# Optimization experiments

Hardware: AMD Instinct MI355X
Metric: run time of the kernel (lower is better)

## Reference

```python
import jax, jax.numpy as jnp
import numpy as np
from functools import partial

# ---- NASA Li-ion battery default parameters (Daigle model) ----
P = {}
P['qMobile'] = 7600.0
P['xnMax'] = 0.6; P['xnMin'] = 0.0
P['xpMax'] = 1.0; P['xpMin'] = 0.4
P['qmax'] = P['qMobile'] / (P['xnMax'] - P['xnMin'])  # 12666.667
P['Ro'] = 0.117215
P['R'] = 8.3144621
P['F'] = 96487.0
P['alpha'] = 0.5
P['Sn'] = 0.000437545
P['Sp'] = 0.00030962
P['kn'] = 2120.96
P['kp'] = 248898.0
P['Volume'] = 2e-5
P['VolumeSurf'] = 0.1
P['tDiffusion'] = 7e6
P['to'] = 6.08671
P['tsn'] = 1001.38
P['tsp'] = 46.4311
P['VolS'] = P['VolumeSurf'] * P['Volume']
P['VolB'] = P['Volume'] - P['VolS']
P['qSMax'] = P['qmax'] * P['VolS'] / P['Volume']
P['qBMax'] = P['qmax'] * P['VolB'] / P['Volume']
U0P, U0N = 4.03, 0.01
APS = np.array([-31593.7, 0.106747, 24606.4, -78561.9, 13317.9, 307387.0,
                84916.1, -1.07469e6, 2285.04, 990894.0, 283920.0, -161513.0,
                -469218.0], dtype=np.float32)
ANS = np.array([86.19], dtype=np.float32)
DT = 1.0
B, T = 2048, 1024


def _vint(x, As, F):
    N = As.shape[0]
    k = jnp.arange(N, dtype=x.dtype)          # [N]
    ki = jnp.arange(N)
    b = (2.0 * x - 1.0)[..., None]            # [B,1]
    ab, sg = jnp.abs(b), jnp.sign(b)
    # integer-exponent pow with correct sign for negative base
    p_kp1 = ab ** (k + 1.0) * jnp.where((ki + 1) % 2 == 1, sg, 1.0)
    p_km1 = ab ** (k - 1.0) * jnp.where((ki - 1) % 2 != 0, sg, 1.0)
    term = p_kp1 - (2.0 * x * (1.0 - x))[..., None] * k * p_km1
    return (term @ As) / F


def _vint_safe(x, As, F):
    ok = x != 0.5
    sx = jnp.where(ok, x, 1.0)
    return jnp.where(ok, _vint(sx, As, F), 0.0)


def _step(state, i, Aps, Ans):
    tb, Vo, Vsn, Vsp, qnB, qnS, qpB, qpS = state
    R, F, alpha = P['R'], P['F'], P['alpha']
    xpS = qpS / P['qSMax']
    xnS = qnS / P['qSMax']
    Jn0 = P['kn'] * (1.0 - xnS) ** alpha * xnS ** alpha
    Jp0 = P['kp'] * (1.0 - xpS) ** alpha * xpS ** alpha
    dBSn = (qnB / P['VolB'] - qnS / P['VolS']) / P['tDiffusion']
    dBSp = (qpB / P['VolB'] - qpS / P['VolS']) / P['tDiffusion']
    Jn, Jp = i / P['Sn'], i / P['Sp']
    VoN = i * P['Ro']
    VsnN = R * tb / (F * alpha) * jnp.arcsinh(Jn / (2.0 * Jn0))
    VspN = R * tb / (F * alpha) * jnp.arcsinh(Jp / (2.0 * Jp0))
    Ven = U0N + R * tb / F * jnp.log((1.0 - xnS) / xnS) + _vint_safe(xnS, Ans, F)
    Vep = U0P + R * tb / F * jnp.log((1.0 - xpS) / xpS) + _vint_safe(xpS, Aps, F)
    v = Vep - Ven - Vo - Vsn - Vsp
    new = (tb,
           Vo + DT * (VoN - Vo) / P['to'],
           Vsn + DT * (VsnN - Vsn) / P['tsn'],
           Vsp + DT * (VspN - Vsp) / P['tsp'],
           qnB - DT * dBSn,
           qnS + DT * (dBSn - i),
           qpB - DT * dBSp,
           qpS + DT * (i + dBSp))
    return new, v


def setup_inputs() -> dict:
    key = jax.random.key(0)
    k1, = jax.random.split(key, 1)
    i = 0.1 + 0.9 * jax.random.uniform(k1, (B, T), dtype=jnp.float32)  # amps
    qnS0 = P['xnMax'] * P['qmax'] * P['VolS'] / P['Volume']
    qnB0 = P['xnMax'] * P['qmax'] * P['VolB'] / P['Volume']
    qpS0 = P['xpMin'] * P['qmax'] * P['VolS'] / P['Volume']
    qpB0 = P['xpMin'] * P['qmax'] * P['VolB'] / P['Volume']
    x0 = jnp.tile(jnp.array([292.1, 0.0, 0.0, 0.0, qnB0, qnS0, qpB0, qpS0],
                            dtype=jnp.float32), (B, 1))
    return {'i': i, 'x0': x0, 'Aps': jnp.asarray(APS), 'Ans': jnp.asarray(ANS)}


def reference(i, x0, Aps, Ans):
    state0 = tuple(x0[:, j] for j in range(8))
    def body(st, it):
        return _step(st, it, Aps, Ans)
    _, v = jax.lax.scan(body, state0, i.T)  # v: [T,B]
    return v.T  # voltage per cell per step, [B,T]
```

## Files before the change

kernel.cpp:

```cpp
#include <hip/hip_runtime.h>
#include <math.h>


constexpr int NTHR = 256;
constexpr int L = 4;
constexpr int NW = NTHR / 64;

__global__ __launch_bounds__(NTHR, 6) void battery_scan2(
    const float* __restrict__ I, const float* __restrict__ X0,
    const float* __restrict__ Aps, const float* __restrict__ Ans,
    float* __restrict__ out, int Tn)
{
    const int cell = blockIdx.x;
    const int tid  = threadIdx.x;
    const int lane = tid & 63;
    const int wv   = tid >> 6;

    __shared__ float shA[3][NW];
    __shared__ float shC[2][NW];

    const float ivB    = (float)(1.0/1.8e-5);
    const float ivS    = (float)(1.0/2.0e-6);
    const float invSum = (float)(1.0/(1.0/1.8e-5 + 1.0/2.0e-6));
    const float aq     = (float)(1.0 - (1.0/1.8e-5 + 1.0/2.0e-6)/7.0e6);
    const float ao     = (float)(1.0 - 1.0/6.08671);
    const float asn    = (float)(1.0 - 1.0/1001.38);
    const float asp    = (float)(1.0 - 1.0/46.4311);
    const float inv_qS = (float)(1.0/1266.6666666666667);
    const float invF   = (float)(1.0/96487.0);
    const float c_zn   = (float)(0.5/0.000437545/2120.96);
    const float c_zp   = (float)(0.5/0.00030962/248898.0);
    const float Ro_to  = (float)(0.117215/6.08671);
    const float inv_tsn= (float)(1.0/1001.38);
    const float inv_tsp= (float)(1.0/46.4311);
    const float U0PN   = 4.03f - 0.01f;

    const float aqp[4]  = {1.f, aq,  aq*aq,   aq*aq*aq};
    const float aop[4]  = {1.f, ao,  ao*ao,   ao*ao*ao};
    const float asnp[4] = {1.f, asn, asn*asn, asn*asn*asn};
    const float aspp[4] = {1.f, asp, asp*asp, asp*asp*asp};
    const float aq4 = aqp[3]*aq, ao4 = aop[3]*ao;
    const float asn4 = asnp[3]*asn, asp4 = aspp[3]*asp;

    const float tb   = X0[cell*8+0];
    const float Vo0  = X0[cell*8+1];
    const float Vsn0 = X0[cell*8+2];
    const float Vsp0 = X0[cell*8+3];
    const float qnB0 = X0[cell*8+4];
    const float qnS0 = X0[cell*8+5];
    const float qpB0 = X0[cell*8+6];
    const float qpS0 = X0[cell*8+7];
    const float An0  = Ans[0];

    const float rtf  = 8.3144621f * tb * invF;
    const float rtfa = 2.f*rtf;
    const float u_n0 = qnB0 + qnS0;
    const float u_p0 = qpB0 + qpS0;
    const float w_n0 = qnB0*ivB - qnS0*ivS;
    const float w_p0 = qpB0*ivB - qpS0*ivS;

    const float fl = (float)lane;
    const float plq  = exp2f(fl * __log2f(aq4));
    const float plo  = exp2f(fl * __log2f(ao4));
    const float pln  = exp2f(fl * __log2f(asn4));
    const float plp  = exp2f(fl * __log2f(asp4));

    const float4 iv4 = *(const float4*)(I + (size_t)cell*Tn + tid*L);
    const float i4[4] = {iv4.x, iv4.y, iv4.z, iv4.w};

    auto wscan = [&](float tot, float R4, float& ep, float& Tw, float& R64) {
        float v = tot, r = R4;
        #pragma unroll
        for (int s = 1; s < 64; s <<= 1) {
            float p = __shfl_up(v, s);
            v = (lane >= s) ? fmaf(r, p, v) : v;
            r *= r;
        }
        float e = __shfl_up(v, 1);
        ep = (lane == 0) ? 0.f : e;
        Tw = __shfl(v, 63);
        R64 = r;
    };

    float es[4], eg[4], eo[4];
    float ts = 0.f, tg = 0.f, to_ = 0.f;
    #pragma unroll
    for (int k = 0; k < L; ++k) {
        es[k] = ts; eg[k] = tg; eo[k] = to_;
        float b = i4[k];
        ts  += b;
        tg   = fmaf(aq, tg, b);
        to_  = fmaf(ao, to_, b);
    }
    float epS, TwS, RS, epG, TwG, RG, epO, TwO, RO;
    wscan(ts,  1.f, epS, TwS, RS);
    wscan(tg,  aq4, epG, TwG, RG);
    wscan(to_, ao4, epO, TwO, RO);
    if (lane == 0) { shA[0][wv] = TwS; shA[1][wv] = TwG; shA[2][wv] = TwO; }
    __syncthreads();
    float Cs = 0.f, Cg = 0.f, Co = 0.f;
    for (int w2 = 0; w2 < wv; ++w2) {
        Cs = Cs + shA[0][w2];
        Cg = fmaf(RG, Cg, 0.f) ; Cg = Cg;
        Co = Co;
        (void)0;
    }
    Cs = 0.f; Cg = 0.f; Co = 0.f;
    for (int w2 = 0; w2 < wv; ++w2) {
        Cs = Cs + shA[0][w2];
        Cg = fmaf(Cg, RG, shA[1][w2]) - Cg*RG + Cg*RG;
        Co = Co*RO + shA[2][w2];
    }
    {
        Cs = 0.f; Cg = 0.f; Co = 0.f;
        #pragma unroll
        for (int w2 = 0; w2 < NW; ++w2) {
            if (w2 < wv) {
                Cs = Cs + shA[0][w2];
                Cg = Cg*RG + shA[1][w2];
                Co = Co*RO + shA[2][w2];
            }
        }
    }
    const float cs = epS + Cs;
    const float cg = fmaf(plq, Cg, epG);
    const float co = fmaf(plo, Co, epO);

    float pwq = plq, pwo = plo;
    for (int w2 = 0; w2 < wv; ++w2) { pwq *= RG; pwo *= RO; }

    float vpart[4], bsn[4], bsp[4];
    float tn_ = 0.f, tp_ = 0.f;
    #pragma unroll
    for (int k = 0; k < L; ++k) {
        float s_t = cs + es[k];
        float g_t = fmaf(aqp[k], cg, eg[k]);
        float o_t = fmaf(aop[k], co, eo[k]);
        float u_n = u_n0 - s_t, u_p = u_p0 + s_t;
        float paq = pwq * aqp[k];
        float w_n = fmaf(paq, w_n0,  ivS*g_t);
        float w_p = fmaf(paq, w_p0, -ivS*g_t);
        float qnS = (u_n*ivB - w_n)*invSum;
        float qpS = (u_p*ivB - w_p)*invSum;
        float xnS = qnS*inv_qS, xpS = qpS*inv_qS;
        float Vo_t = fmaf(pwo*aop[k], Vo0, Ro_to*o_t);
        float it = i4[k];

        float pn = xnS*(1.f - xnS);
        float pp = xpS*(1.f - xpS);
        float zn = it * c_zn * rsqrtf(pn);
        float zp = it * c_zp * rsqrtf(pp);
        float VsnN = rtfa*__logf(zn + sqrtf(fmaf(zn, zn, 1.f)));
        float VspN = rtfa*__logf(zp + sqrtf(fmaf(zp, zp, 1.f)));

        float num = (1.f - xpS)*xnS;
        float den = xpS*(1.f - xnS);
        float lr  = __logf(__fdividef(num, den));

        float bp_ = 2.f*xpS - 1.f;
        float P = 0.f, D = 0.f;
        #pragma unroll
        for (int j = 12; j >= 0; --j) {
            D = fmaf(D, bp_, P);
            P = fmaf(P, bp_, Aps[j]);
        }
        float vint_p = (xpS != 0.5f)
                     ? (bp_*P - 2.f*xpS*(1.f - xpS)*D)*invF : 0.f;
        float bn_ = 2.f*xnS - 1.f;
        float vint_n = (xnS != 0.5f) ? An0*bn_*invF : 0.f;

        vpart[k] = U0PN + rtf*lr + vint_p - vint_n - Vo_t;
        float bn = VsnN * inv_tsn;
        float bpv = VspN * inv_tsp;
        bsn[k] = bn; bsp[k] = bpv;
        tn_ = fmaf(asn, tn_, bn);
        tp_ = fmaf(asp, tp_, bpv);
    }

    float epN, TwN, RN, epP, TwP, RP;
    wscan(tn_, asn4, epN, TwN, RN);
    wscan(tp_, asp4, epP, TwP, RP);
    if (lane == 0) { shC[0][wv] = TwN; shC[1][wv] = TwP; }
    __syncthreads();
    float Cn = 0.f, Cp = 0.f;
    #pragma unroll
    for (int w2 = 0; w2 < NW; ++w2) {
        if (w2 < wv) {
            Cn = Cn*RN + shC[0][w2];
            Cp = Cp*RP + shC[1][w2];
        }
    }
    const float csn = fmaf(pln, Cn, epN);
    const float csp = fmaf(plp, Cp, epP);
    float pwn = pln, pwp = plp;
    for (int w2 = 0; w2 < wv; ++w2) { pwn *= RN; pwp *= RP; }

    float res[4];
    float an_ = 0.f, ap_ = 0.f;
    #pragma unroll
    for (int k = 0; k < L; ++k) {
        float Vsn_t = fmaf(pwn*asnp[k], Vsn0, fmaf(asnp[k], csn, an_));
        float Vsp_t = fmaf(pwp*aspp[k], Vsp0, fmaf(aspp[k], csp, ap_));
        res[k] = vpart[k] - Vsn_t - Vsp_t;
        an_ = fmaf(asn, an_, bsn[k]);
        ap_ = fmaf(asp, ap_, bsp[k]);
    }
    *(float4*)(out + (size_t)cell*Tn + tid*L) = make_float4(res[0],res[1],res[2],res[3]);
}

extern "C" void kernel_launch(void* const* d_in, const int* in_sizes, int n_in,
                              void* d_out, int out_size, void* d_ws, size_t ws_size,
                              hipStream_t stream) {
    const float* I   = (const float*)d_in[0];
    const float* X0  = (const float*)d_in[1];
    const float* Aps = (const float*)d_in[2];
    const float* Ans = (const float*)d_in[3];
    float* out = (float*)d_out;

    int Bn = in_sizes[1] / 8;
    int Tn = in_sizes[0] / Bn;

    battery_scan2<<<dim3(Bn), dim3(NTHR), 0, stream>>>(I, X0, Aps, Ans, out, Tn);
}
```

Before: 74.66 us.

## Use 128-thread blocks with 8 steps per thread and incremental decay recurrences

Each block now covers a cell's 1024 steps with 2 waves instead of 4, and each thread handles 8 timesteps. That halves the number of shuffle-based wave scans per element and reduces the cross-wave combine to a single branch. Per-step decay powers are now updated by running multiplication instead of precomputed tables, and several constants are folded together. The positive-electrode arcsinh is replaced by a cubic Taylor series, which assumes the argument stays small. Longer serial chains per thread and higher register pressure may lower latency hiding.

```diff
diff --git a/kernel.cpp b/kernel.cpp
--- a/kernel.cpp
+++ b/kernel.cpp
@@ -2,11 +2,10 @@
 #include <math.h>
 
 
-constexpr int NTHR = 256;
-constexpr int L = 4;
-constexpr int NW = NTHR / 64;
+constexpr int NTHR = 128;
+constexpr int L = 8;
 
-__global__ __launch_bounds__(NTHR, 6) void battery_scan2(
+__global__ __launch_bounds__(NTHR, 4) void battery_scan3(
     const float* __restrict__ I, const float* __restrict__ X0,
     const float* __restrict__ Aps, const float* __restrict__ Ans,
     float* __restrict__ out, int Tn)
@@ -16,31 +15,27 @@
     const int lane = tid & 63;
     const int wv   = tid >> 6;
 
-    __shared__ float shA[3][NW];
-    __shared__ float shC[2][NW];
+    __shared__ float shA[3][2];
+    __shared__ float shC[2][2];
 
     const float ivB    = (float)(1.0/1.8e-5);
     const float ivS    = (float)(1.0/2.0e-6);
-    const float invSum = (float)(1.0/(1.0/1.8e-5 + 1.0/2.0e-6));
     const float aq     = (float)(1.0 - (1.0/1.8e-5 + 1.0/2.0e-6)/7.0e6);
     const float ao     = (float)(1.0 - 1.0/6.08671);
     const float asn    = (float)(1.0 - 1.0/1001.38);
     const float asp    = (float)(1.0 - 1.0/46.4311);
-    const float inv_qS = (float)(1.0/1266.6666666666667);
+    const float invSum = (float)(1.0/(1.0/1.8e-5 + 1.0/2.0e-6));
+    const float cX     = (float)((1.0/(1.0/1.8e-5 + 1.0/2.0e-6)) / 1266.6666666666667);
     const float invF   = (float)(1.0/96487.0);
     const float c_zn   = (float)(0.5/0.000437545/2120.96);
     const float c_zp   = (float)(0.5/0.00030962/248898.0);
     const float Ro_to  = (float)(0.117215/6.08671);
-    const float inv_tsn= (float)(1.0/1001.38);
-    const float inv_tsp= (float)(1.0/46.4311);
     const float U0PN   = 4.03f - 0.01f;
 
-    const float aqp[4]  = {1.f, aq,  aq*aq,   aq*aq*aq};
-    const float aop[4]  = {1.f, ao,  ao*ao,   ao*ao*ao};
-    const float asnp[4] = {1.f, asn, asn*asn, asn*asn*asn};
-    const float aspp[4] = {1.f, asp, asp*asp, asp*asp*asp};
-    const float aq4 = aqp[3]*aq, ao4 = aop[3]*ao;
-    const float asn4 = asnp[3]*asn, asp4 = aspp[3]*asp;
+    float aqp = 1.f, aop = 1.f, asnp = 1.f, aspp = 1.f;
+    #pragma unroll
+    for (int k = 0; k < L; ++k) { aqp *= aq; aop *= ao; asnp *= asn; aspp *= asp; }
+    const float aqL = aqp, aoL = aop, asnL = asnp, aspL = aspp;
 
     const float tb   = X0[cell*8+0];
     const float Vo0  = X0[cell*8+1];
@@ -50,26 +45,30 @@
     const float qnS0 = X0[cell*8+5];
     const float qpB0 = X0[cell*8+6];
     const float qpS0 = X0[cell*8+7];
-    const float An0  = Ans[0];
+    const float An0F = Ans[0] * invF;
 
-    const float rtf  = 8.3144621f * tb * invF;
-    const float rtfa = 2.f*rtf;
-    const float u_n0 = qnB0 + qnS0;
-    const float u_p0 = qpB0 + qpS0;
-    const float w_n0 = qnB0*ivB - qnS0*ivS;
-    const float w_p0 = qpB0*ivB - qpS0*ivS;
+    const float rtf   = 8.3144621f * tb * invF;
+    const float rtfa  = 2.f*rtf;
+    const float bn_c  = rtfa * (float)(1.0/1001.38);
+    const float bp_c  = rtfa * (float)(1.0/46.4311);
+    const float u_n0  = qnB0 + qnS0;
+    const float u_p0  = qpB0 + qpS0;
+    const float w_n0  = qnB0*ivB - qnS0*ivS;
+    const float w_p0  = qpB0*ivB - qpS0*ivS;
 
     const float fl = (float)lane;
-    const float plq  = exp2f(fl * __log2f(aq4));
-    const float plo  = exp2f(fl * __log2f(ao4));
-    const float pln  = exp2f(fl * __log2f(asn4));
-    const float plp  = exp2f(fl * __log2f(asp4));
+    const float plq = exp2f(fl * __log2f(aqL));
+    const float plo = exp2f(fl * __log2f(aoL));
+    const float pln = exp2f(fl * __log2f(asnL));
+    const float plp = exp2f(fl * __log2f(aspL));
 
-    const float4 iv4 = *(const float4*)(I + (size_t)cell*Tn + tid*L);
-    const float i4[4] = {iv4.x, iv4.y, iv4.z, iv4.w};
+    const float* ibase = I + (size_t)cell*Tn + tid*L;
+    const float4 iva = *(const float4*)(ibase);
+    const float4 ivb = *(const float4*)(ibase + 4);
+    const float i8[8] = {iva.x, iva.y, iva.z, iva.w, ivb.x, ivb.y, ivb.z, ivb.w};
 
-    auto wscan = [&](float tot, float R4, float& ep, float& Tw, float& R64) {
-        float v = tot, r = R4;
+    auto wscan = [&](float tot, float RL, float& ep, float& Tw, float& R64) {
+        float v = tot, r = RL;
         #pragma unroll
         for (int s = 1; s < 64; s <<= 1) {
             float p = __shfl_up(v, s);
@@ -82,130 +81,100 @@
         R64 = r;
     };
 
-    float es[4], eg[4], eo[4];
     float ts = 0.f, tg = 0.f, to_ = 0.f;
     #pragma unroll
     for (int k = 0; k < L; ++k) {
-        es[k] = ts; eg[k] = tg; eo[k] = to_;
-        float b = i4[k];
-        ts  += b;
-        tg   = fmaf(aq, tg, b);
-        to_  = fmaf(ao, to_, b);
+        float b = i8[k];
+        ts += b; tg = fmaf(aq, tg, b); to_ = fmaf(ao, to_, b);
     }
     float epS, TwS, RS, epG, TwG, RG, epO, TwO, RO;
     wscan(ts,  1.f, epS, TwS, RS);
-    wscan(tg,  aq4, epG, TwG, RG);
-    wscan(to_, ao4, epO, TwO, RO);
+    wscan(tg,  aqL, epG, TwG, RG);
+    wscan(to_, aoL, epO, TwO, RO);
     if (lane == 0) { shA[0][wv] = TwS; shA[1][wv] = TwG; shA[2][wv] = TwO; }
     __syncthreads();
-    float Cs = 0.f, Cg = 0.f, Co = 0.f;
-    for (int w2 = 0; w2 < wv; ++w2) {
-        Cs = Cs + shA[0][w2];
-        Cg = fmaf(RG, Cg, 0.f) ; Cg = Cg;
-        Co = Co;
-        (void)0;
+    float cs = epS, cg = epG, co = epO;
+    float pwq = plq, pwo = plo;
+    if (wv) {
+        cs += shA[0][0];
+        cg = fmaf(plq, shA[1][0], cg);
+        co = fmaf(plo, shA[2][0], co);
+        pwq *= RG; pwo *= RO;
     }
-    Cs = 0.f; Cg = 0.f; Co = 0.f;
-    for (int w2 = 0; w2 < wv; ++w2) {
-        Cs = Cs + shA[0][w2];
-        Cg = fmaf(Cg, RG, shA[1][w2]) - Cg*RG + Cg*RG;
-        Co = Co*RO + shA[2][w2];
-    }
-    {
-        Cs = 0.f; Cg = 0.f; Co = 0.f;
-        #pragma unroll
-        for (int w2 = 0; w2 < NW; ++w2) {
-            if (w2 < wv) {
-                Cs = Cs + shA[0][w2];
-                Cg = Cg*RG + shA[1][w2];
-                Co = Co*RO + shA[2][w2];
-            }
-        }
-    }
-    const float cs = epS + Cs;
-    const float cg = fmaf(plq, Cg, epG);
-    const float co = fmaf(plo, Co, epO);
 
-    float pwq = plq, pwo = plo;
-    for (int w2 = 0; w2 < wv; ++w2) { pwq *= RG; pwo *= RO; }
-
-    float vpart[4], bsn[4], bsp[4];
-    float tn_ = 0.f, tp_ = 0.f;
+    float vpart[L], bsn[L], bsp[L];
+    float S = cs, G = cg, O = co;
+    float hwn = pwq*w_n0, hwp = pwq*w_p0;
+    float hvo = pwo*Vo0;
+    float rn = 0.f, rp = 0.f;
     #pragma unroll
     for (int k = 0; k < L; ++k) {
-        float s_t = cs + es[k];
-        float g_t = fmaf(aqp[k], cg, eg[k]);
-        float o_t = fmaf(aop[k], co, eo[k]);
-        float u_n = u_n0 - s_t, u_p = u_p0 + s_t;
-        float paq = pwq * aqp[k];
-        float w_n = fmaf(paq, w_n0,  ivS*g_t);
-        float w_p = fmaf(paq, w_p0, -ivS*g_t);
-        float qnS = (u_n*ivB - w_n)*invSum;
-        float qpS = (u_p*ivB - w_p)*invSum;
-        float xnS = qnS*inv_qS, xpS = qpS*inv_qS;
-        float Vo_t = fmaf(pwo*aop[k], Vo0, Ro_to*o_t);
-        float it = i4[k];
+        float it  = i8[k];
+        float u_n = u_n0 - S, u_p = u_p0 + S;
+        float w_n = fmaf( ivS, G, hwn);
+        float w_p = fmaf(-ivS, G, hwp);
+        float xnS = (fmaf(u_n, ivB, -w_n)) * cX;
+        float xpS = (fmaf(u_p, ivB, -w_p)) * cX;
+        float Vo_t = fmaf(Ro_to, O, hvo);
+        S += it; G = fmaf(aq, G, it); O = fmaf(ao, O, it);
+        hwn *= aq; hwp *= aq; hvo *= ao;
 
-        float pn = xnS*(1.f - xnS);
-        float pp = xpS*(1.f - xpS);
+        float pn = fmaf(-xnS, xnS, xnS);
+        float pp = fmaf(-xpS, xpS, xpS);
         float zn = it * c_zn * rsqrtf(pn);
         float zp = it * c_zp * rsqrtf(pp);
-        float VsnN = rtfa*__logf(zn + sqrtf(fmaf(zn, zn, 1.f)));
-        float VspN = rtfa*__logf(zp + sqrtf(fmaf(zp, zp, 1.f)));
+        float asn_n = __logf(zn + sqrtf(fmaf(zn, zn, 1.f)));
+        float zp2  = zp*zp;
+        float asn_p = zp * fmaf(-0.16666667f, zp2, 1.f);
+        bsn[k] = bn_c * asn_n;
+        bsp[k] = bp_c * asn_p;
+        rn = fmaf(asn, rn, bsn[k]);
+        rp = fmaf(asp, rp, bsp[k]);
 
-        float num = (1.f - xpS)*xnS;
-        float den = xpS*(1.f - xnS);
-        float lr  = __logf(__fdividef(num, den));
+        float omxn = 1.f - xnS, omxp = 1.f - xpS;
+        float lr = __logf(__fdividef(omxp * xnS, xpS * omxn));
 
-        float bp_ = 2.f*xpS - 1.f;
+        float b_ = fmaf(2.f, xpS, -1.f);
         float P = 0.f, D = 0.f;
         #pragma unroll
         for (int j = 12; j >= 0; --j) {
-            D = fmaf(D, bp_, P);
-            P = fmaf(P, bp_, Aps[j]);
+            D = fmaf(D, b_, P);
+            P = fmaf(P, b_, Aps[j]);
         }
-        float vint_p = (xpS != 0.5f)
-                     ? (bp_*P - 2.f*xpS*(1.f - xpS)*D)*invF : 0.f;
-        float bn_ = 2.f*xnS - 1.f;
-        float vint_n = (xnS != 0.5f) ? An0*bn_*invF : 0.f;
+        float pp2 = pp + pp;
+        float vint_p = (b_*P - pp2*D) * invF;
+        vint_p = (xpS != 0.5f) ? vint_p : 0.f;
+        float vint_n = An0F * fmaf(2.f, xnS, -1.f);
 
-        vpart[k] = U0PN + rtf*lr + vint_p - vint_n - Vo_t;
-        float bn = VsnN * inv_tsn;
-        float bpv = VspN * inv_tsp;
-        bsn[k] = bn; bsp[k] = bpv;
-        tn_ = fmaf(asn, tn_, bn);
-        tp_ = fmaf(asp, tp_, bpv);
+        vpart[k] = U0PN + fmaf(rtf, lr, vint_p - vint_n - Vo_t);
     }
 
     float epN, TwN, RN, epP, TwP, RP;
-    wscan(tn_, asn4, epN, TwN, RN);
-    wscan(tp_, asp4, epP, TwP, RP);
+    wscan(rn, asnL, epN, TwN, RN);
+    wscan(rp, aspL, epP, TwP, RP);
     if (lane == 0) { shC[0][wv] = TwN; shC[1][wv] = TwP; }
     __syncthreads();
-    float Cn = 0.f, Cp = 0.f;
-    #pragma unroll
-    for (int w2 = 0; w2 < NW; ++w2) {
-        if (w2 < wv) {
-            Cn = Cn*RN + shC[0][w2];
-            Cp = Cp*RP + shC[1][w2];
-        }
+    float csn = epN, csp = epP;
+    float pwn = pln, pwp = plp;
+    if (wv) {
+        csn = fmaf(pln, shC[0][0], csn);
+        csp = fmaf(plp, shC[1][0], csp);
+        pwn *= RN; pwp *= RP;
     }
-    const float csn = fmaf(pln, Cn, epN);
-    const float csp = fmaf(plp, Cp, epP);
-    float pwn = pln, pwp = plp;
-    for (int w2 = 0; w2 < wv; ++w2) { pwn *= RN; pwp *= RP; }
 
-    float res[4];
-    float an_ = 0.f, ap_ = 0.f;
+    float N = csn, Pv = csp;
+    float hn = pwn*Vsn0, hp = pwp*Vsp0;
     #pragma unroll
     for (int k = 0; k < L; ++k) {
-        float Vsn_t = fmaf(pwn*asnp[k], Vsn0, fmaf(asnp[k], csn, an_));
-        float Vsp_t = fmaf(pwp*aspp[k], Vsp0, fmaf(aspp[k], csp, ap_));
-        res[k] = vpart[k] - Vsn_t - Vsp_t;
-        an_ = fmaf(asn, an_, bsn[k]);
-        ap_ = fmaf(asp, ap_, bsp[k]);
+        vpart[k] -= (hn + N) + (hp + Pv);
+        N  = fmaf(asn, N,  bsn[k]);
+        Pv = fmaf(asp, Pv, bsp[k]);
+        hn *= asn; hp *= asp;
     }
-    *(float4*)(out + (size_t)cell*Tn + tid*L) = make_float4(res[0],res[1],res[2],res[3]);
+
+    float* obase = out + (size_t)cell*Tn + tid*L;
+    *(float4*)(obase)     = make_float4(vpart[0], vpart[1], vpart[2], vpart[3]);
+    *(float4*)(obase + 4) = make_float4(vpart[4], vpart[5], vpart[6], vpart[7]);
 }
 
 extern "C" void kernel_launch(void* const* d_in, const int* in_sizes, int n_in,
@@ -220,5 +189,5 @@
     int Bn = in_sizes[1] / 8;
     int Tn = in_sizes[0] / Bn;
 
-    battery_scan2<<<dim3(Bn), dim3(NTHR), 0, stream>>>(I, X0, Aps, Ans, out, Tn);
+    battery_scan3<<<dim3(Bn), dim3(NTHR), 0, stream>>>(I, X0, Aps, Ans, out, Tn);
 }
```

After: 73.12 us. -2.1%, faster.
